# Performance work log

Hardware: AMD Instinct MI355X
Metric: run time of the kernel (lower is better)

Reference implementation:

```python
import jax, jax.numpy as jnp
import numpy as np

E, D, H, K, N = 8, 512, 2048, 2, 1024  # experts, d_model, d_hidden, top_k, tokens
EPS = 1e-5


def _moe_linear(x, idx, W, b):
    # x: (M, in); idx: (M,) expert id per row; W: (E, out, in); b: (E, out)
    # Brute-force: compute per-expert dense GEMMs, select via one-hot (matches
    # BruteForceMoELinear math: y[i] = x[i] @ W[idx[i]].T + b[idx[i]]).
    m = jax.nn.one_hot(idx, W.shape[0], dtype=x.dtype)  # (M, E)
    y = jnp.einsum('me,eoi,mi->mo', m, W, x)
    return y + jnp.take(b, idx, axis=0)


def _forward(inp, gate_w, gate_b, w1, b1, w2, b2, ln_w, ln_b):
    # NaiveGate: linear -> top_k -> softmax over top-k logits
    logits = inp @ gate_w.T + gate_b              # (N, E)
    top_val, top_idx = jax.lax.top_k(logits, K)   # (N, K)
    score = jax.nn.softmax(top_val, axis=-1)      # (N, K)
    # repeat_interleave tokens, dispatch to experts
    x = jnp.repeat(inp, K, axis=0)                # (N*K, D)
    idx = top_idx.reshape(-1)                     # (N*K,)
    x = _moe_linear(x, idx, w1, b1)               # (N*K, H)
    x = jax.nn.gelu(x, approximate=False)         # torch F.gelu default = erf
    x = _moe_linear(x, idx, w2, b2)               # (N*K, D)
    x = x.reshape(N, K, D)
    x = jnp.einsum('nk,nkd->nd', score, x)        # bmm((N,1,K),(N,K,D)) combine
    # post layer norm (pre_lnorm=False)
    mu = jnp.mean(x, axis=-1, keepdims=True)
    var = jnp.var(x, axis=-1, keepdims=True)
    return (x - mu) * jax.lax.rsqrt(var + EPS) * ln_w + ln_b


def setup_inputs() -> dict:
    key = jax.random.key(0)
    ks = jax.random.split(key, 8)
    s = 0.02
    return {
        'inp': jax.random.normal(ks[0], (N, D), dtype=jnp.float32),
        'gate_w': s * jax.random.normal(ks[1], (E, D), dtype=jnp.float32),
        'gate_b': jnp.zeros((E,), dtype=jnp.float32),
        'w1': s * jax.random.normal(ks[2], (E, H, D), dtype=jnp.float32),
        'b1': jnp.zeros((E, H), dtype=jnp.float32),
        'w2': s * jax.random.normal(ks[3], (E, D, H), dtype=jnp.float32),
        'b2': jnp.zeros((E, D), dtype=jnp.float32),
        'ln_w': jnp.ones((D,), dtype=jnp.float32),
        'ln_b': jnp.zeros((D,), dtype=jnp.float32),
    }


def reference(inp, gate_w, gate_b, w1, b1, w2, b2, ln_w, ln_b):
    return _forward(inp, gate_w, gate_b, w1, b1, w2, b2, ln_w, ln_b)
```

## Files before the change

kernel.cpp:

```cpp
#include <hip/hip_runtime.h>
#include <cstdint>
#include <cstddef>

typedef _Float16 half_t;
typedef _Float16 half8 __attribute__((ext_vector_type(8)));
typedef float floatx4 __attribute__((ext_vector_type(4)));

#define E_ 8
#define D_ 512
#define H_ 2048
#define NTOK 1024
#define NP 2048
#define TM 128
#define MAX_TILES 24

__device__ __forceinline__ float gelu_f(float x) {
    return 0.5f * x * (1.0f + erff(x * 0.7071067811865476f));
}

__device__ __forceinline__ void gload_lds16(const half_t* g, half_t* l) {
    __builtin_amdgcn_global_load_lds(
        (__attribute__((address_space(1))) void*)(g),
        (__attribute__((address_space(3))) void*)(l),
        16, 0, 0);
}

__global__ __launch_bounds__(256) void gate_kernel(
        const float* __restrict__ inp, const float* __restrict__ gate_w,
        const float* __restrict__ gate_b, float* __restrict__ logits) {
    int n = blockIdx.x * 4 + (threadIdx.x >> 6);
    int lane = threadIdx.x & 63;
    const floatx4* xr = (const floatx4*)(inp + (size_t)n * D_);
    floatx4 x0 = xr[lane * 2], x1 = xr[lane * 2 + 1];
    #pragma unroll
    for (int e = 0; e < E_; e++) {
        const floatx4* gr = (const floatx4*)(gate_w + (size_t)e * D_);
        floatx4 g0 = gr[lane * 2], g1 = gr[lane * 2 + 1];
        float p = x0[0]*g0[0] + x0[1]*g0[1] + x0[2]*g0[2] + x0[3]*g0[3]
                + x1[0]*g1[0] + x1[1]*g1[1] + x1[2]*g1[2] + x1[3]*g1[3];
        #pragma unroll
        for (int m = 1; m < 64; m <<= 1) p += __shfl_xor(p, m);
        if (lane == 0) logits[(size_t)n * E_ + e] = p + gate_b[e];
    }
}

__global__ __launch_bounds__(256) void plan_kernel(
        const float* __restrict__ logits, float* __restrict__ score,
        int* __restrict__ idx, int* __restrict__ pos_of_pair,
        int* __restrict__ tile_e, int* __restrict__ tile_row0,
        int* __restrict__ tile_cnt, int* __restrict__ ntiles) {
    __shared__ int cnt_s[E_], off_s[E_ + 1], cur_s[E_];
    int tid = threadIdx.x;
    if (tid < E_) { cnt_s[tid] = 0; cur_s[tid] = 0; }
    __syncthreads();
    int my_e[4][2];
    #pragma unroll
    for (int i = 0; i < 4; i++) {
        int n = tid + i * 256;
        float l[E_];
        #pragma unroll
        for (int e = 0; e < E_; e++) l[e] = logits[(size_t)n * E_ + e];
        int e0 = 0; float v0 = l[0];
        #pragma unroll
        for (int e = 1; e < E_; e++) if (l[e] > v0) { v0 = l[e]; e0 = e; }
        int e1 = -1; float v1 = -3.4e38f;
        #pragma unroll
        for (int e = 0; e < E_; e++) if (e != e0 && l[e] > v1) { v1 = l[e]; e1 = e; }
        float s1 = expf(v1 - v0);
        float den = 1.0f + s1;
        score[2 * n]     = 1.0f / den;
        score[2 * n + 1] = s1 / den;
        idx[2 * n]     = e0;
        idx[2 * n + 1] = e1;
        atomicAdd(&cnt_s[e0], 1);
        atomicAdd(&cnt_s[e1], 1);
        my_e[i][0] = e0; my_e[i][1] = e1;
    }
    __syncthreads();
    if (tid == 0) {
        int o = 0;
        #pragma unroll
        for (int e = 0; e < E_; e++) { off_s[e] = o; o += cnt_s[e]; }
        off_s[E_] = o;
        int t = 0;
        for (int e = 0; e < E_; e++) {
            int c = cnt_s[e];
            int nt = (c + TM - 1) / TM;
            for (int i = 0; i < nt; i++) {
                tile_e[t] = e;
                tile_row0[t] = off_s[e] + i * TM;
                int rem = c - i * TM;
                tile_cnt[t] = rem < TM ? rem : TM;
                t++;
            }
        }
        ntiles[0] = t;
    }
    __syncthreads();
    #pragma unroll
    for (int i = 0; i < 4; i++) {
        #pragma unroll
        for (int k = 0; k < 2; k++) {
            int p = (tid + i * 256) * 2 + k;
            int e = my_e[i][k];
            int r = atomicAdd(&cur_s[e], 1);
            pos_of_pair[p] = off_s[e] + r;
        }
    }
}

__global__ __launch_bounds__(256) void scatter_kernel(
        const float* __restrict__ inp, const int* __restrict__ pos_of_pair,
        half_t* __restrict__ Xg) {
    int p = blockIdx.x * 4 + (threadIdx.x >> 6);
    int lane = threadIdx.x & 63;
    int pos = pos_of_pair[p];
    int n = p >> 1;
    const floatx4* src = (const floatx4*)(inp + (size_t)n * D_);
    floatx4 f0 = src[lane * 2], f1 = src[lane * 2 + 1];
    half8 h = { (half_t)f0[0], (half_t)f0[1], (half_t)f0[2], (half_t)f0[3],
                (half_t)f1[0], (half_t)f1[1], (half_t)f1[2], (half_t)f1[3] };
    *(half8*)(Xg + (size_t)pos * D_ + lane * 8) = h;
}

__global__ __launch_bounds__(256) void cvt_kernel(
        const float* __restrict__ w1, const float* __restrict__ w2,
        half_t* __restrict__ W1h, half_t* __restrict__ W2h) {
    const int n8 = E_ * H_ * D_ / 8;
    int i = blockIdx.x * 256 + threadIdx.x;
    const float* src; half_t* dst; int j;
    if (i < n8) { src = w1; dst = W1h; j = i; }
    else        { src = w2; dst = W2h; j = i - n8; }
    const floatx4* s = (const floatx4*)src + (size_t)j * 2;
    floatx4 f0 = s[0], f1 = s[1];
    half8 h = { (half_t)f0[0], (half_t)f0[1], (half_t)f0[2], (half_t)f0[3],
                (half_t)f1[0], (half_t)f1[1], (half_t)f1[2], (half_t)f1[3] };
    *(half8*)(dst + (size_t)j * 8) = h;
}

__global__ __launch_bounds__(256) void gemm1_kernel(
        const half_t* __restrict__ Xg, const half_t* __restrict__ W1h,
        const float* __restrict__ b1,
        const int* __restrict__ tile_e, const int* __restrict__ tile_row0,
        const int* __restrict__ tile_cnt, const int* __restrict__ ntiles,
        half_t* __restrict__ Y1) {
    __shared__ half_t As[TM * 32];
    __shared__ half_t Bs[128 * 32];
    int t = blockIdx.x;
    if (t >= ntiles[0]) return;
    int e = tile_e[t], row0 = tile_row0[t], cnt = tile_cnt[t];
    int colbase = blockIdx.y * 128;
    int tid = threadIdx.x;
    int wave = tid >> 6, lane = tid & 63;
    int quad = lane >> 4, l16 = lane & 15;
    int wm = (wave & 1) * 64, wn = (wave >> 1) * 64;

    int acol = (tid & 3) * 8;
    const half_t* Ag0 = Xg + (size_t)(row0 + (tid >> 2)) * D_ + acol;
    const half_t* Ag1 = Ag0 + 64 * D_;
    const half_t* Bg0 = W1h + ((size_t)e * H_ + colbase + (tid >> 2)) * D_ + acol;
    const half_t* Bg1 = Bg0 + 64 * D_;
    half_t* la0 = As + tid * 8;
    half_t* la1 = As + (tid + 256) * 8;
    half_t* lb0 = Bs + tid * 8;
    half_t* lb1 = Bs + (tid + 256) * 8;

    floatx4 acc[4][4] = {};
    for (int k0 = 0; k0 < D_; k0 += 32) {
        __syncthreads();
        gload_lds16(Ag0 + k0, la0);
        gload_lds16(Ag1 + k0, la1);
        gload_lds16(Bg0 + k0, lb0);
        gload_lds16(Bg1 + k0, lb1);
        __syncthreads();
        half8 a[4], b[4];
        #pragma unroll
        for (int mi = 0; mi < 4; mi++)
            a[mi] = *(const half8*)(As + (wm + mi * 16 + l16) * 32 + quad * 8);
        #pragma unroll
        for (int ni = 0; ni < 4; ni++)
            b[ni] = *(const half8*)(Bs + (wn + ni * 16 + l16) * 32 + quad * 8);
        #pragma unroll
        for (int mi = 0; mi < 4; mi++)
            #pragma unroll
            for (int ni = 0; ni < 4; ni++)
                acc[mi][ni] = __builtin_amdgcn_mfma_f32_16x16x32_f16(a[mi], b[ni], acc[mi][ni], 0, 0, 0);
    }
    float bias[4];
    #pragma unroll
    for (int ni = 0; ni < 4; ni++)
        bias[ni] = b1[(size_t)e * H_ + colbase + wn + ni * 16 + l16];
    #pragma unroll
    for (int mi = 0; mi < 4; mi++) {
        #pragma unroll
        for (int r = 0; r < 4; r++) {
            int rr = wm + mi * 16 + quad * 4 + r;
            if (rr >= cnt) continue;
            size_t rowoff = (size_t)(row0 + rr) * H_;
            #pragma unroll
            for (int ni = 0; ni < 4; ni++) {
                float v = acc[mi][ni][r] + bias[ni];
                Y1[rowoff + colbase + wn + ni * 16 + l16] = (half_t)gelu_f(v);
            }
        }
    }
}

__global__ __launch_bounds__(256) void gemm2_kernel(
        const half_t* __restrict__ Y1, const half_t* __restrict__ W2h,
        const int* __restrict__ tile_e, const int* __restrict__ tile_row0,
        const int* __restrict__ tile_cnt, const int* __restrict__ ntiles,
        float* __restrict__ Y2p) {
    __shared__ half_t As[TM * 32];
    __shared__ half_t Bs[128 * 32];
    int t = blockIdx.x;
    if (t >= ntiles[0]) return;
    int e = tile_e[t], row0 = tile_row0[t], cnt = tile_cnt[t];
    int colbase = blockIdx.y * 128;
    int kz = blockIdx.z;
    int kzbase = kz * 512;
    int tid = threadIdx.x;
    int wave = tid >> 6, lane = tid & 63;
    int quad = lane >> 4, l16 = lane & 15;
    int wm = (wave & 1) * 64, wn = (wave >> 1) * 64;

    int acol = (tid & 3) * 8;
    const half_t* Ag0 = Y1 + (size_t)(row0 + (tid >> 2)) * H_ + kzbase + acol;
    const half_t* Ag1 = Ag0 + 64 * H_;
    const half_t* Bg0 = W2h + ((size_t)e * D_ + colbase + (tid >> 2)) * H_ + kzbase + acol;
    const half_t* Bg1 = Bg0 + 64 * H_;
    half_t* la0 = As + tid * 8;
    half_t* la1 = As + (tid + 256) * 8;
    half_t* lb0 = Bs + tid * 8;
    half_t* lb1 = Bs + (tid + 256) * 8;

    floatx4 acc[4][4] = {};
    for (int k0 = 0; k0 < 512; k0 += 32) {
        __syncthreads();
        gload_lds16(Ag0 + k0, la0);
        gload_lds16(Ag1 + k0, la1);
        gload_lds16(Bg0 + k0, lb0);
        gload_lds16(Bg1 + k0, lb1);
        __syncthreads();
        half8 a[4], b[4];
        #pragma unroll
        for (int mi = 0; mi < 4; mi++)
            a[mi] = *(const half8*)(As + (wm + mi * 16 + l16) * 32 + quad * 8);
        #pragma unroll
        for (int ni = 0; ni < 4; ni++)
            b[ni] = *(const half8*)(Bs + (wn + ni * 16 + l16) * 32 + quad * 8);
        #pragma unroll
        for (int mi = 0; mi < 4; mi++)
            #pragma unroll
            for (int ni = 0; ni < 4; ni++)
                acc[mi][ni] = __builtin_amdgcn_mfma_f32_16x16x32_f16(a[mi], b[ni], acc[mi][ni], 0, 0, 0);
    }
    #pragma unroll
    for (int mi = 0; mi < 4; mi++) {
        #pragma unroll
        for (int r = 0; r < 4; r++) {
            int rr = wm + mi * 16 + quad * 4 + r;
            if (rr >= cnt) continue;
            size_t rowoff = ((size_t)kz * NP + row0 + rr) * D_;
            #pragma unroll
            for (int ni = 0; ni < 4; ni++)
                Y2p[rowoff + colbase + wn + ni * 16 + l16] = acc[mi][ni][r];
        }
    }
}

__global__ __launch_bounds__(256) void final_kernel(
        const float* __restrict__ Y2p, const float* __restrict__ b2,
        const int* __restrict__ idx, const float* __restrict__ score,
        const int* __restrict__ pos_of_pair,
        const float* __restrict__ ln_w, const float* __restrict__ ln_b,
        float* __restrict__ out) {
    int n = blockIdx.x * 4 + (threadIdx.x >> 6);
    int lane = threadIdx.x & 63;
    int p0 = pos_of_pair[2 * n], p1 = pos_of_pair[2 * n + 1];
    int e0 = idx[2 * n], e1 = idx[2 * n + 1];
    float s0 = score[2 * n], s1 = score[2 * n + 1];

    const floatx4* b2r0 = (const floatx4*)(b2 + (size_t)e0 * D_);
    const floatx4* b2r1 = (const floatx4*)(b2 + (size_t)e1 * D_);
    floatx4 a_lo = b2r0[lane * 2], a_hi = b2r0[lane * 2 + 1];
    floatx4 c_lo = b2r1[lane * 2], c_hi = b2r1[lane * 2 + 1];
    #pragma unroll
    for (int kz = 0; kz < 4; kz++) {
        const floatx4* r0 = (const floatx4*)(Y2p + ((size_t)kz * NP + p0) * D_);
        const floatx4* r1 = (const floatx4*)(Y2p + ((size_t)kz * NP + p1) * D_);
        a_lo += r0[lane * 2]; a_hi += r0[lane * 2 + 1];
        c_lo += r1[lane * 2]; c_hi += r1[lane * 2 + 1];
    }
    floatx4 y_lo = s0 * a_lo + s1 * c_lo;
    floatx4 y_hi = s0 * a_hi + s1 * c_hi;

    float s = 0.0f, q = 0.0f;
    #pragma unroll
    for (int j = 0; j < 4; j++) {
        s += y_lo[j] + y_hi[j];
        q += y_lo[j] * y_lo[j] + y_hi[j] * y_hi[j];
    }
    #pragma unroll
    for (int m = 1; m < 64; m <<= 1) {
        s += __shfl_xor(s, m);
        q += __shfl_xor(q, m);
    }
    float mean = s * (1.0f / 512.0f);
    float var = q * (1.0f / 512.0f) - mean * mean;
    float inv = 1.0f / sqrtf(var + 1e-5f);

    const floatx4* wv = (const floatx4*)ln_w;
    const floatx4* bv = (const floatx4*)ln_b;
    floatx4 o_lo = (y_lo - mean) * inv * wv[lane * 2]     + bv[lane * 2];
    floatx4 o_hi = (y_hi - mean) * inv * wv[lane * 2 + 1] + bv[lane * 2 + 1];
    floatx4* op = (floatx4*)(out + (size_t)n * D_);
    op[lane * 2] = o_lo;
    op[lane * 2 + 1] = o_hi;
}

extern "C" void kernel_launch(void* const* d_in, const int* in_sizes, int n_in,
                              void* d_out, int out_size, void* d_ws, size_t ws_size,
                              hipStream_t stream) {
    const float* inp    = (const float*)d_in[0];
    const float* gate_w = (const float*)d_in[1];
    const float* gate_b = (const float*)d_in[2];
    const float* w1     = (const float*)d_in[3];
    const float* b1     = (const float*)d_in[4];
    const float* w2     = (const float*)d_in[5];
    const float* b2     = (const float*)d_in[6];
    const float* ln_w   = (const float*)d_in[7];
    const float* ln_b   = (const float*)d_in[8];
    float* out = (float*)d_out;

    char* ws = (char*)d_ws;
    size_t o = 0;
    auto carve = [&](size_t bytes) -> char* {
        char* p = ws + o;
        o += (bytes + 255) & ~(size_t)255;
        return p;
    };
    half_t* W1h = (half_t*)carve(sizeof(half_t) * (size_t)E_ * H_ * D_);
    half_t* W2h = (half_t*)carve(sizeof(half_t) * (size_t)E_ * D_ * H_);
    half_t* Xg  = (half_t*)carve(sizeof(half_t) * (size_t)(NP + TM) * D_);
    half_t* Y1  = (half_t*)carve(sizeof(half_t) * (size_t)(NP + TM) * H_);
    float*  Y2p = (float*)carve(sizeof(float) * 4 * (size_t)NP * D_);
    float*  logits = (float*)carve(sizeof(float) * NTOK * E_);
    float*  score  = (float*)carve(sizeof(float) * NP);
    int* idx         = (int*)carve(sizeof(int) * NP);
    int* pos_of_pair = (int*)carve(sizeof(int) * NP);
    int* tile_e      = (int*)carve(sizeof(int) * MAX_TILES);
    int* tile_row0   = (int*)carve(sizeof(int) * MAX_TILES);
    int* tile_cnt    = (int*)carve(sizeof(int) * MAX_TILES);
    int* ntiles      = (int*)carve(sizeof(int) * 1);

    gate_kernel<<<NTOK / 4, 256, 0, stream>>>(inp, gate_w, gate_b, logits);
    plan_kernel<<<1, 256, 0, stream>>>(logits, score, idx, pos_of_pair,
                                       tile_e, tile_row0, tile_cnt, ntiles);
    scatter_kernel<<<NP / 4, 256, 0, stream>>>(inp, pos_of_pair, Xg);
    cvt_kernel<<<2 * E_ * H_ * D_ / 8 / 256, 256, 0, stream>>>(w1, w2, W1h, W2h);
    gemm1_kernel<<<dim3(MAX_TILES, H_ / 128), 256, 0, stream>>>(
        Xg, W1h, b1, tile_e, tile_row0, tile_cnt, ntiles, Y1);
    gemm2_kernel<<<dim3(MAX_TILES, D_ / 128, 4), 256, 0, stream>>>(
        Y1, W2h, tile_e, tile_row0, tile_cnt, ntiles, Y2p);
    final_kernel<<<NTOK / 4, 256, 0, stream>>>(Y2p, b2, idx, score, pos_of_pair, ln_w, ln_b, out);
}
```

Measured before the change: 170.1 us.

## Fuse MoE pipeline into one cooperative persistent kernel with grid syncs

Replaces the seven separate launches (gate, plan, scatter, weight conversion, two grouped GEMMs, combine+layernorm) with a single cooperative kernel that loops over work in grid-stride fashion and separates stages with grid.sync(). The gate and top-2 selection are fused per token, and weight conversion runs in the same phase. The GEMM inner loops now stage 64-wide K chunks in doubled LDS buffers, halving the barriers per tile. The aim is to remove launch gaps and tail effects between small kernels, at the cost of grid-wide barrier overhead, a grid capped at 512 blocks, and a single-block planning phase that leaves most CUs idle.

```diff
diff --git a/kernel.cpp b/kernel.cpp
--- a/kernel.cpp
+++ b/kernel.cpp
@@ -1,6 +1,9 @@
 #include <hip/hip_runtime.h>
+#include <hip/hip_cooperative_groups.h>
 #include <cstdint>
 #include <cstddef>
+
+namespace cg = cooperative_groups;
 
 typedef _Float16 half_t;
 typedef _Float16 half8 __attribute__((ext_vector_type(8)));
@@ -14,6 +17,14 @@
 #define TM 128
 #define MAX_TILES 24
 
+struct Params {
+    const float *inp, *gate_w, *gate_b, *w1, *b1, *w2, *b2, *ln_w, *ln_b;
+    float *out;
+    half_t *W1h, *W2h, *Xg, *Y1;
+    float *Y2p, *score;
+    int *idx, *pos, *tile_e, *tile_row0, *tile_cnt, *ntiles;
+};
+
 __device__ __forceinline__ float gelu_f(float x) {
     return 0.5f * x * (1.0f + erff(x * 0.7071067811865476f));
 }
@@ -25,171 +36,51 @@
         16, 0, 0);
 }
 
-__global__ __launch_bounds__(256) void gate_kernel(
-        const float* __restrict__ inp, const float* __restrict__ gate_w,
-        const float* __restrict__ gate_b, float* __restrict__ logits) {
-    int n = blockIdx.x * 4 + (threadIdx.x >> 6);
-    int lane = threadIdx.x & 63;
-    const floatx4* xr = (const floatx4*)(inp + (size_t)n * D_);
-    floatx4 x0 = xr[lane * 2], x1 = xr[lane * 2 + 1];
-    #pragma unroll
-    for (int e = 0; e < E_; e++) {
-        const floatx4* gr = (const floatx4*)(gate_w + (size_t)e * D_);
-        floatx4 g0 = gr[lane * 2], g1 = gr[lane * 2 + 1];
-        float p = x0[0]*g0[0] + x0[1]*g0[1] + x0[2]*g0[2] + x0[3]*g0[3]
-                + x1[0]*g1[0] + x1[1]*g1[1] + x1[2]*g1[2] + x1[3]*g1[3];
-        #pragma unroll
-        for (int m = 1; m < 64; m <<= 1) p += __shfl_xor(p, m);
-        if (lane == 0) logits[(size_t)n * E_ + e] = p + gate_b[e];
-    }
-}
-
-__global__ __launch_bounds__(256) void plan_kernel(
-        const float* __restrict__ logits, float* __restrict__ score,
-        int* __restrict__ idx, int* __restrict__ pos_of_pair,
-        int* __restrict__ tile_e, int* __restrict__ tile_row0,
-        int* __restrict__ tile_cnt, int* __restrict__ ntiles) {
-    __shared__ int cnt_s[E_], off_s[E_ + 1], cur_s[E_];
-    int tid = threadIdx.x;
-    if (tid < E_) { cnt_s[tid] = 0; cur_s[tid] = 0; }
-    __syncthreads();
-    int my_e[4][2];
-    #pragma unroll
-    for (int i = 0; i < 4; i++) {
-        int n = tid + i * 256;
-        float l[E_];
-        #pragma unroll
-        for (int e = 0; e < E_; e++) l[e] = logits[(size_t)n * E_ + e];
-        int e0 = 0; float v0 = l[0];
-        #pragma unroll
-        for (int e = 1; e < E_; e++) if (l[e] > v0) { v0 = l[e]; e0 = e; }
-        int e1 = -1; float v1 = -3.4e38f;
-        #pragma unroll
-        for (int e = 0; e < E_; e++) if (e != e0 && l[e] > v1) { v1 = l[e]; e1 = e; }
-        float s1 = expf(v1 - v0);
-        float den = 1.0f + s1;
-        score[2 * n]     = 1.0f / den;
-        score[2 * n + 1] = s1 / den;
-        idx[2 * n]     = e0;
-        idx[2 * n + 1] = e1;
-        atomicAdd(&cnt_s[e0], 1);
-        atomicAdd(&cnt_s[e1], 1);
-        my_e[i][0] = e0; my_e[i][1] = e1;
-    }
-    __syncthreads();
-    if (tid == 0) {
-        int o = 0;
-        #pragma unroll
-        for (int e = 0; e < E_; e++) { off_s[e] = o; o += cnt_s[e]; }
-        off_s[E_] = o;
-        int t = 0;
-        for (int e = 0; e < E_; e++) {
-            int c = cnt_s[e];
-            int nt = (c + TM - 1) / TM;
-            for (int i = 0; i < nt; i++) {
-                tile_e[t] = e;
-                tile_row0[t] = off_s[e] + i * TM;
-                int rem = c - i * TM;
-                tile_cnt[t] = rem < TM ? rem : TM;
-                t++;
+__device__ void gemm1_job(const Params& P, half_t* As, half_t* Bs,
+                          int t, int cb, int tid) {
+    int e = P.tile_e[t], row0 = P.tile_row0[t], cnt = P.tile_cnt[t];
+    int colbase = cb * 128;
+    int wave = tid >> 6, lane = tid & 63, quad = lane >> 4, l16 = lane & 15;
+    int wm = (wave & 1) * 64, wn = (wave >> 1) * 64;
+    const half_t* Abase = P.Xg + (size_t)row0 * D_;
+    const half_t* Bbase = P.W1h + ((size_t)e * H_ + colbase) * D_;
+    int srow = tid >> 2, scol = (tid & 3) * 8;
+    floatx4 acc[4][4] = {};
+    for (int k0 = 0; k0 < D_; k0 += 64) {
+        __syncthreads();
+        #pragma unroll
+        for (int j = 0; j < 2; j++) {
+            #pragma unroll
+            for (int s = 0; s < 2; s++) {
+                int q = tid + s * 256;
+                int row = srow + s * 64;
+                gload_lds16(Abase + (size_t)row * D_ + k0 + j * 32 + scol,
+                            As + j * 4096 + q * 8);
+                gload_lds16(Bbase + (size_t)row * D_ + k0 + j * 32 + scol,
+                            Bs + j * 4096 + q * 8);
             }
         }
-        ntiles[0] = t;
-    }
-    __syncthreads();
-    #pragma unroll
-    for (int i = 0; i < 4; i++) {
-        #pragma unroll
-        for (int k = 0; k < 2; k++) {
-            int p = (tid + i * 256) * 2 + k;
-            int e = my_e[i][k];
-            int r = atomicAdd(&cur_s[e], 1);
-            pos_of_pair[p] = off_s[e] + r;
-        }
-    }
-}
-
-__global__ __launch_bounds__(256) void scatter_kernel(
-        const float* __restrict__ inp, const int* __restrict__ pos_of_pair,
-        half_t* __restrict__ Xg) {
-    int p = blockIdx.x * 4 + (threadIdx.x >> 6);
-    int lane = threadIdx.x & 63;
-    int pos = pos_of_pair[p];
-    int n = p >> 1;
-    const floatx4* src = (const floatx4*)(inp + (size_t)n * D_);
-    floatx4 f0 = src[lane * 2], f1 = src[lane * 2 + 1];
-    half8 h = { (half_t)f0[0], (half_t)f0[1], (half_t)f0[2], (half_t)f0[3],
-                (half_t)f1[0], (half_t)f1[1], (half_t)f1[2], (half_t)f1[3] };
-    *(half8*)(Xg + (size_t)pos * D_ + lane * 8) = h;
-}
-
-__global__ __launch_bounds__(256) void cvt_kernel(
-        const float* __restrict__ w1, const float* __restrict__ w2,
-        half_t* __restrict__ W1h, half_t* __restrict__ W2h) {
-    const int n8 = E_ * H_ * D_ / 8;
-    int i = blockIdx.x * 256 + threadIdx.x;
-    const float* src; half_t* dst; int j;
-    if (i < n8) { src = w1; dst = W1h; j = i; }
-    else        { src = w2; dst = W2h; j = i - n8; }
-    const floatx4* s = (const floatx4*)src + (size_t)j * 2;
-    floatx4 f0 = s[0], f1 = s[1];
-    half8 h = { (half_t)f0[0], (half_t)f0[1], (half_t)f0[2], (half_t)f0[3],
-                (half_t)f1[0], (half_t)f1[1], (half_t)f1[2], (half_t)f1[3] };
-    *(half8*)(dst + (size_t)j * 8) = h;
-}
-
-__global__ __launch_bounds__(256) void gemm1_kernel(
-        const half_t* __restrict__ Xg, const half_t* __restrict__ W1h,
-        const float* __restrict__ b1,
-        const int* __restrict__ tile_e, const int* __restrict__ tile_row0,
-        const int* __restrict__ tile_cnt, const int* __restrict__ ntiles,
-        half_t* __restrict__ Y1) {
-    __shared__ half_t As[TM * 32];
-    __shared__ half_t Bs[128 * 32];
-    int t = blockIdx.x;
-    if (t >= ntiles[0]) return;
-    int e = tile_e[t], row0 = tile_row0[t], cnt = tile_cnt[t];
-    int colbase = blockIdx.y * 128;
-    int tid = threadIdx.x;
-    int wave = tid >> 6, lane = tid & 63;
-    int quad = lane >> 4, l16 = lane & 15;
-    int wm = (wave & 1) * 64, wn = (wave >> 1) * 64;
-
-    int acol = (tid & 3) * 8;
-    const half_t* Ag0 = Xg + (size_t)(row0 + (tid >> 2)) * D_ + acol;
-    const half_t* Ag1 = Ag0 + 64 * D_;
-    const half_t* Bg0 = W1h + ((size_t)e * H_ + colbase + (tid >> 2)) * D_ + acol;
-    const half_t* Bg1 = Bg0 + 64 * D_;
-    half_t* la0 = As + tid * 8;
-    half_t* la1 = As + (tid + 256) * 8;
-    half_t* lb0 = Bs + tid * 8;
-    half_t* lb1 = Bs + (tid + 256) * 8;
-
-    floatx4 acc[4][4] = {};
-    for (int k0 = 0; k0 < D_; k0 += 32) {
-        __syncthreads();
-        gload_lds16(Ag0 + k0, la0);
-        gload_lds16(Ag1 + k0, la1);
-        gload_lds16(Bg0 + k0, lb0);
-        gload_lds16(Bg1 + k0, lb1);
-        __syncthreads();
-        half8 a[4], b[4];
-        #pragma unroll
-        for (int mi = 0; mi < 4; mi++)
-            a[mi] = *(const half8*)(As + (wm + mi * 16 + l16) * 32 + quad * 8);
-        #pragma unroll
-        for (int ni = 0; ni < 4; ni++)
-            b[ni] = *(const half8*)(Bs + (wn + ni * 16 + l16) * 32 + quad * 8);
-        #pragma unroll
-        for (int mi = 0; mi < 4; mi++)
+        __syncthreads();
+        #pragma unroll
+        for (int j = 0; j < 2; j++) {
+            half8 a[4], b[4];
+            #pragma unroll
+            for (int mi = 0; mi < 4; mi++)
+                a[mi] = *(const half8*)(As + j * 4096 + (wm + mi * 16 + l16) * 32 + quad * 8);
             #pragma unroll
             for (int ni = 0; ni < 4; ni++)
-                acc[mi][ni] = __builtin_amdgcn_mfma_f32_16x16x32_f16(a[mi], b[ni], acc[mi][ni], 0, 0, 0);
+                b[ni] = *(const half8*)(Bs + j * 4096 + (wn + ni * 16 + l16) * 32 + quad * 8);
+            #pragma unroll
+            for (int mi = 0; mi < 4; mi++)
+                #pragma unroll
+                for (int ni = 0; ni < 4; ni++)
+                    acc[mi][ni] = __builtin_amdgcn_mfma_f32_16x16x32_f16(a[mi], b[ni], acc[mi][ni], 0, 0, 0);
+        }
     }
     float bias[4];
     #pragma unroll
     for (int ni = 0; ni < 4; ni++)
-        bias[ni] = b1[(size_t)e * H_ + colbase + wn + ni * 16 + l16];
+        bias[ni] = P.b1[(size_t)e * H_ + colbase + wn + ni * 16 + l16];
     #pragma unroll
     for (int mi = 0; mi < 4; mi++) {
         #pragma unroll
@@ -200,60 +91,53 @@
             #pragma unroll
             for (int ni = 0; ni < 4; ni++) {
                 float v = acc[mi][ni][r] + bias[ni];
-                Y1[rowoff + colbase + wn + ni * 16 + l16] = (half_t)gelu_f(v);
+                P.Y1[rowoff + colbase + wn + ni * 16 + l16] = (half_t)gelu_f(v);
             }
         }
     }
 }
 
-__global__ __launch_bounds__(256) void gemm2_kernel(
-        const half_t* __restrict__ Y1, const half_t* __restrict__ W2h,
-        const int* __restrict__ tile_e, const int* __restrict__ tile_row0,
-        const int* __restrict__ tile_cnt, const int* __restrict__ ntiles,
-        float* __restrict__ Y2p) {
-    __shared__ half_t As[TM * 32];
-    __shared__ half_t Bs[128 * 32];
-    int t = blockIdx.x;
-    if (t >= ntiles[0]) return;
-    int e = tile_e[t], row0 = tile_row0[t], cnt = tile_cnt[t];
-    int colbase = blockIdx.y * 128;
-    int kz = blockIdx.z;
-    int kzbase = kz * 512;
-    int tid = threadIdx.x;
-    int wave = tid >> 6, lane = tid & 63;
-    int quad = lane >> 4, l16 = lane & 15;
+__device__ void gemm2_job(const Params& P, half_t* As, half_t* Bs,
+                          int t, int cb, int kz, int tid) {
+    int e = P.tile_e[t], row0 = P.tile_row0[t], cnt = P.tile_cnt[t];
+    int colbase = cb * 128;
+    int kzb = kz * 512;
+    int wave = tid >> 6, lane = tid & 63, quad = lane >> 4, l16 = lane & 15;
     int wm = (wave & 1) * 64, wn = (wave >> 1) * 64;
-
-    int acol = (tid & 3) * 8;
-    const half_t* Ag0 = Y1 + (size_t)(row0 + (tid >> 2)) * H_ + kzbase + acol;
-    const half_t* Ag1 = Ag0 + 64 * H_;
-    const half_t* Bg0 = W2h + ((size_t)e * D_ + colbase + (tid >> 2)) * H_ + kzbase + acol;
-    const half_t* Bg1 = Bg0 + 64 * H_;
-    half_t* la0 = As + tid * 8;
-    half_t* la1 = As + (tid + 256) * 8;
-    half_t* lb0 = Bs + tid * 8;
-    half_t* lb1 = Bs + (tid + 256) * 8;
-
+    const half_t* Abase = P.Y1 + (size_t)row0 * H_ + kzb;
+    const half_t* Bbase = P.W2h + ((size_t)e * D_ + colbase) * H_ + kzb;
+    int srow = tid >> 2, scol = (tid & 3) * 8;
     floatx4 acc[4][4] = {};
-    for (int k0 = 0; k0 < 512; k0 += 32) {
-        __syncthreads();
-        gload_lds16(Ag0 + k0, la0);
-        gload_lds16(Ag1 + k0, la1);
-        gload_lds16(Bg0 + k0, lb0);
-        gload_lds16(Bg1 + k0, lb1);
-        __syncthreads();
-        half8 a[4], b[4];
-        #pragma unroll
-        for (int mi = 0; mi < 4; mi++)
-            a[mi] = *(const half8*)(As + (wm + mi * 16 + l16) * 32 + quad * 8);
-        #pragma unroll
-        for (int ni = 0; ni < 4; ni++)
-            b[ni] = *(const half8*)(Bs + (wn + ni * 16 + l16) * 32 + quad * 8);
-        #pragma unroll
-        for (int mi = 0; mi < 4; mi++)
+    for (int k0 = 0; k0 < 512; k0 += 64) {
+        __syncthreads();
+        #pragma unroll
+        for (int j = 0; j < 2; j++) {
+            #pragma unroll
+            for (int s = 0; s < 2; s++) {
+                int q = tid + s * 256;
+                int row = srow + s * 64;
+                gload_lds16(Abase + (size_t)row * H_ + k0 + j * 32 + scol,
+                            As + j * 4096 + q * 8);
+                gload_lds16(Bbase + (size_t)row * H_ + k0 + j * 32 + scol,
+                            Bs + j * 4096 + q * 8);
+            }
+        }
+        __syncthreads();
+        #pragma unroll
+        for (int j = 0; j < 2; j++) {
+            half8 a[4], b[4];
+            #pragma unroll
+            for (int mi = 0; mi < 4; mi++)
+                a[mi] = *(const half8*)(As + j * 4096 + (wm + mi * 16 + l16) * 32 + quad * 8);
             #pragma unroll
             for (int ni = 0; ni < 4; ni++)
-                acc[mi][ni] = __builtin_amdgcn_mfma_f32_16x16x32_f16(a[mi], b[ni], acc[mi][ni], 0, 0, 0);
+                b[ni] = *(const half8*)(Bs + j * 4096 + (wn + ni * 16 + l16) * 32 + quad * 8);
+            #pragma unroll
+            for (int mi = 0; mi < 4; mi++)
+                #pragma unroll
+                for (int ni = 0; ni < 4; ni++)
+                    acc[mi][ni] = __builtin_amdgcn_mfma_f32_16x16x32_f16(a[mi], b[ni], acc[mi][ni], 0, 0, 0);
+        }
     }
     #pragma unroll
     for (int mi = 0; mi < 4; mi++) {
@@ -264,75 +148,178 @@
             size_t rowoff = ((size_t)kz * NP + row0 + rr) * D_;
             #pragma unroll
             for (int ni = 0; ni < 4; ni++)
-                Y2p[rowoff + colbase + wn + ni * 16 + l16] = acc[mi][ni][r];
-        }
-    }
-}
-
-__global__ __launch_bounds__(256) void final_kernel(
-        const float* __restrict__ Y2p, const float* __restrict__ b2,
-        const int* __restrict__ idx, const float* __restrict__ score,
-        const int* __restrict__ pos_of_pair,
-        const float* __restrict__ ln_w, const float* __restrict__ ln_b,
-        float* __restrict__ out) {
-    int n = blockIdx.x * 4 + (threadIdx.x >> 6);
-    int lane = threadIdx.x & 63;
-    int p0 = pos_of_pair[2 * n], p1 = pos_of_pair[2 * n + 1];
-    int e0 = idx[2 * n], e1 = idx[2 * n + 1];
-    float s0 = score[2 * n], s1 = score[2 * n + 1];
-
-    const floatx4* b2r0 = (const floatx4*)(b2 + (size_t)e0 * D_);
-    const floatx4* b2r1 = (const floatx4*)(b2 + (size_t)e1 * D_);
-    floatx4 a_lo = b2r0[lane * 2], a_hi = b2r0[lane * 2 + 1];
-    floatx4 c_lo = b2r1[lane * 2], c_hi = b2r1[lane * 2 + 1];
-    #pragma unroll
-    for (int kz = 0; kz < 4; kz++) {
-        const floatx4* r0 = (const floatx4*)(Y2p + ((size_t)kz * NP + p0) * D_);
-        const floatx4* r1 = (const floatx4*)(Y2p + ((size_t)kz * NP + p1) * D_);
-        a_lo += r0[lane * 2]; a_hi += r0[lane * 2 + 1];
-        c_lo += r1[lane * 2]; c_hi += r1[lane * 2 + 1];
-    }
-    floatx4 y_lo = s0 * a_lo + s1 * c_lo;
-    floatx4 y_hi = s0 * a_hi + s1 * c_hi;
-
-    float s = 0.0f, q = 0.0f;
-    #pragma unroll
-    for (int j = 0; j < 4; j++) {
-        s += y_lo[j] + y_hi[j];
-        q += y_lo[j] * y_lo[j] + y_hi[j] * y_hi[j];
-    }
-    #pragma unroll
-    for (int m = 1; m < 64; m <<= 1) {
-        s += __shfl_xor(s, m);
-        q += __shfl_xor(q, m);
-    }
-    float mean = s * (1.0f / 512.0f);
-    float var = q * (1.0f / 512.0f) - mean * mean;
-    float inv = 1.0f / sqrtf(var + 1e-5f);
-
-    const floatx4* wv = (const floatx4*)ln_w;
-    const floatx4* bv = (const floatx4*)ln_b;
-    floatx4 o_lo = (y_lo - mean) * inv * wv[lane * 2]     + bv[lane * 2];
-    floatx4 o_hi = (y_hi - mean) * inv * wv[lane * 2 + 1] + bv[lane * 2 + 1];
-    floatx4* op = (floatx4*)(out + (size_t)n * D_);
-    op[lane * 2] = o_lo;
-    op[lane * 2 + 1] = o_hi;
+                P.Y2p[rowoff + colbase + wn + ni * 16 + l16] = acc[mi][ni][r];
+        }
+    }
+}
+
+__global__ __launch_bounds__(256, 2) void moe_mega(Params P) {
+    cg::grid_group grid = cg::this_grid();
+    __shared__ __align__(16) char smem[32768];
+    half_t* As = (half_t*)smem;
+    half_t* Bs = As + 8192;
+    const int blk = blockIdx.x, tid = threadIdx.x;
+    const int wave = tid >> 6, lane = tid & 63;
+    const int gstride = gridDim.x;
+
+    for (int n = blk * 4 + wave; n < NTOK; n += gstride * 4) {
+        const floatx4* xr = (const floatx4*)(P.inp + (size_t)n * D_);
+        floatx4 x0 = xr[lane * 2], x1 = xr[lane * 2 + 1];
+        float l[E_];
+        #pragma unroll
+        for (int e = 0; e < E_; e++) {
+            const floatx4* gr = (const floatx4*)(P.gate_w + (size_t)e * D_);
+            floatx4 g0 = gr[lane * 2], g1 = gr[lane * 2 + 1];
+            float p = x0[0]*g0[0] + x0[1]*g0[1] + x0[2]*g0[2] + x0[3]*g0[3]
+                    + x1[0]*g1[0] + x1[1]*g1[1] + x1[2]*g1[2] + x1[3]*g1[3];
+            #pragma unroll
+            for (int m = 1; m < 64; m <<= 1) p += __shfl_xor(p, m);
+            l[e] = p + P.gate_b[e];
+        }
+        if (lane == 0) {
+            int e0 = 0; float v0 = l[0];
+            #pragma unroll
+            for (int e = 1; e < E_; e++) if (l[e] > v0) { v0 = l[e]; e0 = e; }
+            int e1 = -1; float v1 = -3.4e38f;
+            #pragma unroll
+            for (int e = 0; e < E_; e++) if (e != e0 && l[e] > v1) { v1 = l[e]; e1 = e; }
+            float s1 = expf(v1 - v0);
+            float den = 1.0f + s1;
+            P.score[2 * n]     = 1.0f / den;
+            P.score[2 * n + 1] = s1 / den;
+            P.idx[2 * n]     = e0;
+            P.idx[2 * n + 1] = e1;
+        }
+    }
+    {
+        const int NG = E_ * H_ * D_ / 8;
+        for (int i = blk * 256 + tid; i < 2 * NG; i += gstride * 256) {
+            const float* src; half_t* dst; int j;
+            if (i < NG) { src = P.w1; dst = P.W1h; j = i; }
+            else        { src = P.w2; dst = P.W2h; j = i - NG; }
+            const floatx4* s = (const floatx4*)src + (size_t)j * 2;
+            floatx4 f0 = s[0], f1 = s[1];
+            half8 h = { (half_t)f0[0], (half_t)f0[1], (half_t)f0[2], (half_t)f0[3],
+                        (half_t)f1[0], (half_t)f1[1], (half_t)f1[2], (half_t)f1[3] };
+            *(half8*)(dst + (size_t)j * 8) = h;
+        }
+    }
+    grid.sync();
+
+    if (blk == 0) {
+        int* cnt_s = (int*)smem;
+        int* off_s = cnt_s + E_;
+        int* cur_s = off_s + E_ + 1;
+        if (tid < E_) { cnt_s[tid] = 0; cur_s[tid] = 0; }
+        __syncthreads();
+        int my_e[8];
+        #pragma unroll
+        for (int i = 0; i < 8; i++) {
+            my_e[i] = P.idx[tid * 8 + i];
+            atomicAdd(&cnt_s[my_e[i]], 1);
+        }
+        __syncthreads();
+        if (tid == 0) {
+            int o = 0;
+            #pragma unroll
+            for (int e = 0; e < E_; e++) { off_s[e] = o; o += cnt_s[e]; }
+            off_s[E_] = o;
+            int t = 0;
+            for (int e = 0; e < E_; e++) {
+                int c = cnt_s[e];
+                int ntt = (c + TM - 1) / TM;
+                for (int i = 0; i < ntt; i++) {
+                    P.tile_e[t] = e;
+                    P.tile_row0[t] = off_s[e] + i * TM;
+                    int rem = c - i * TM;
+                    P.tile_cnt[t] = rem < TM ? rem : TM;
+                    t++;
+                }
+            }
+            P.ntiles[0] = t;
+        }
+        __syncthreads();
+        #pragma unroll
+        for (int i = 0; i < 8; i++) {
+            int e = my_e[i];
+            int r = atomicAdd(&cur_s[e], 1);
+            P.pos[tid * 8 + i] = off_s[e] + r;
+        }
+    }
+    grid.sync();
+
+    for (int p = blk * 4 + wave; p < NP; p += gstride * 4) {
+        int pos = P.pos[p];
+        int n = p >> 1;
+        const floatx4* src = (const floatx4*)(P.inp + (size_t)n * D_);
+        floatx4 f0 = src[lane * 2], f1 = src[lane * 2 + 1];
+        half8 h = { (half_t)f0[0], (half_t)f0[1], (half_t)f0[2], (half_t)f0[3],
+                    (half_t)f1[0], (half_t)f1[1], (half_t)f1[2], (half_t)f1[3] };
+        *(half8*)(P.Xg + (size_t)pos * D_ + lane * 8) = h;
+    }
+    grid.sync();
+
+    {
+        int nt = P.ntiles[0];
+        for (int job = blk; job < nt * 16; job += gstride)
+            gemm1_job(P, As, Bs, job >> 4, job & 15, tid);
+    }
+    grid.sync();
+
+    {
+        int nt = P.ntiles[0];
+        for (int job = blk; job < nt * 16; job += gstride)
+            gemm2_job(P, As, Bs, job >> 4, (job >> 2) & 3, job & 3, tid);
+    }
+    grid.sync();
+
+    for (int n = blk * 4 + wave; n < NTOK; n += gstride * 4) {
+        int p0 = P.pos[2 * n], p1 = P.pos[2 * n + 1];
+        int e0 = P.idx[2 * n], e1 = P.idx[2 * n + 1];
+        float s0 = P.score[2 * n], s1 = P.score[2 * n + 1];
+
+        const floatx4* b2r0 = (const floatx4*)(P.b2 + (size_t)e0 * D_);
+        const floatx4* b2r1 = (const floatx4*)(P.b2 + (size_t)e1 * D_);
+        floatx4 a_lo = b2r0[lane * 2], a_hi = b2r0[lane * 2 + 1];
+        floatx4 c_lo = b2r1[lane * 2], c_hi = b2r1[lane * 2 + 1];
+        #pragma unroll
+        for (int kz = 0; kz < 4; kz++) {
+            const floatx4* r0 = (const floatx4*)(P.Y2p + ((size_t)kz * NP + p0) * D_);
+            const floatx4* r1 = (const floatx4*)(P.Y2p + ((size_t)kz * NP + p1) * D_);
+            a_lo += r0[lane * 2]; a_hi += r0[lane * 2 + 1];
+            c_lo += r1[lane * 2]; c_hi += r1[lane * 2 + 1];
+        }
+        floatx4 y_lo = s0 * a_lo + s1 * c_lo;
+        floatx4 y_hi = s0 * a_hi + s1 * c_hi;
+
+        float s = 0.0f, q = 0.0f;
+        #pragma unroll
+        for (int j = 0; j < 4; j++) {
+            s += y_lo[j] + y_hi[j];
+            q += y_lo[j] * y_lo[j] + y_hi[j] * y_hi[j];
+        }
+        #pragma unroll
+        for (int m = 1; m < 64; m <<= 1) {
+            s += __shfl_xor(s, m);
+            q += __shfl_xor(q, m);
+        }
+        float mean = s * (1.0f / 512.0f);
+        float var = q * (1.0f / 512.0f) - mean * mean;
+        float inv = 1.0f / sqrtf(var + 1e-5f);
+
+        const floatx4* wv = (const floatx4*)P.ln_w;
+        const floatx4* bv = (const floatx4*)P.ln_b;
+        floatx4 o_lo = (y_lo - mean) * inv * wv[lane * 2]     + bv[lane * 2];
+        floatx4 o_hi = (y_hi - mean) * inv * wv[lane * 2 + 1] + bv[lane * 2 + 1];
+        floatx4* op = (floatx4*)(P.out + (size_t)n * D_);
+        op[lane * 2] = o_lo;
+        op[lane * 2 + 1] = o_hi;
+    }
 }
 
 extern "C" void kernel_launch(void* const* d_in, const int* in_sizes, int n_in,
                               void* d_out, int out_size, void* d_ws, size_t ws_size,
                               hipStream_t stream) {
-    const float* inp    = (const float*)d_in[0];
-    const float* gate_w = (const float*)d_in[1];
-    const float* gate_b = (const float*)d_in[2];
-    const float* w1     = (const float*)d_in[3];
-    const float* b1     = (const float*)d_in[4];
-    const float* w2     = (const float*)d_in[5];
-    const float* b2     = (const float*)d_in[6];
-    const float* ln_w   = (const float*)d_in[7];
-    const float* ln_b   = (const float*)d_in[8];
-    float* out = (float*)d_out;
-
     char* ws = (char*)d_ws;
     size_t o = 0;
     auto carve = [&](size_t bytes) -> char* {
@@ -340,28 +327,37 @@
         o += (bytes + 255) & ~(size_t)255;
         return p;
     };
-    half_t* W1h = (half_t*)carve(sizeof(half_t) * (size_t)E_ * H_ * D_);
-    half_t* W2h = (half_t*)carve(sizeof(half_t) * (size_t)E_ * D_ * H_);
-    half_t* Xg  = (half_t*)carve(sizeof(half_t) * (size_t)(NP + TM) * D_);
-    half_t* Y1  = (half_t*)carve(sizeof(half_t) * (size_t)(NP + TM) * H_);
-    float*  Y2p = (float*)carve(sizeof(float) * 4 * (size_t)NP * D_);
-    float*  logits = (float*)carve(sizeof(float) * NTOK * E_);
-    float*  score  = (float*)carve(sizeof(float) * NP);
-    int* idx         = (int*)carve(sizeof(int) * NP);
-    int* pos_of_pair = (int*)carve(sizeof(int) * NP);
-    int* tile_e      = (int*)carve(sizeof(int) * MAX_TILES);
-    int* tile_row0   = (int*)carve(sizeof(int) * MAX_TILES);
-    int* tile_cnt    = (int*)carve(sizeof(int) * MAX_TILES);
-    int* ntiles      = (int*)carve(sizeof(int) * 1);
-
-    gate_kernel<<<NTOK / 4, 256, 0, stream>>>(inp, gate_w, gate_b, logits);
-    plan_kernel<<<1, 256, 0, stream>>>(logits, score, idx, pos_of_pair,
-                                       tile_e, tile_row0, tile_cnt, ntiles);
-    scatter_kernel<<<NP / 4, 256, 0, stream>>>(inp, pos_of_pair, Xg);
-    cvt_kernel<<<2 * E_ * H_ * D_ / 8 / 256, 256, 0, stream>>>(w1, w2, W1h, W2h);
-    gemm1_kernel<<<dim3(MAX_TILES, H_ / 128), 256, 0, stream>>>(
-        Xg, W1h, b1, tile_e, tile_row0, tile_cnt, ntiles, Y1);
-    gemm2_kernel<<<dim3(MAX_TILES, D_ / 128, 4), 256, 0, stream>>>(
-        Y1, W2h, tile_e, tile_row0, tile_cnt, ntiles, Y2p);
-    final_kernel<<<NTOK / 4, 256, 0, stream>>>(Y2p, b2, idx, score, pos_of_pair, ln_w, ln_b, out);
-}
+    Params P;
+    P.inp    = (const float*)d_in[0];
+    P.gate_w = (const float*)d_in[1];
+    P.gate_b = (const float*)d_in[2];
+    P.w1     = (const float*)d_in[3];
+    P.b1     = (const float*)d_in[4];
+    P.w2     = (const float*)d_in[5];
+    P.b2     = (const float*)d_in[6];
+    P.ln_w   = (const float*)d_in[7];
+    P.ln_b   = (const float*)d_in[8];
+    P.out    = (float*)d_out;
+    P.W1h = (half_t*)carve(sizeof(half_t) * (size_t)E_ * H_ * D_);
+    P.W2h = (half_t*)carve(sizeof(half_t) * (size_t)E_ * D_ * H_);
+    P.Xg  = (half_t*)carve(sizeof(half_t) * (size_t)(NP + TM) * D_);
+    P.Y1  = (half_t*)carve(sizeof(half_t) * (size_t)(NP + TM) * H_);
+    P.Y2p = (float*)carve(sizeof(float) * 4 * (size_t)NP * D_);
+    P.score = (float*)carve(sizeof(float) * NP);
+    P.idx   = (int*)carve(sizeof(int) * NP);
+    P.pos   = (int*)carve(sizeof(int) * NP);
+    P.tile_e    = (int*)carve(sizeof(int) * MAX_TILES);
+    P.tile_row0 = (int*)carve(sizeof(int) * MAX_TILES);
+    P.tile_cnt  = (int*)carve(sizeof(int) * MAX_TILES);
+    P.ntiles    = (int*)carve(sizeof(int) * 1);
+
+    int occ = 0;
+    hipOccupancyMaxActiveBlocksPerMultiprocessor(&occ, moe_mega, 256, 0);
+    if (occ < 1) occ = 1;
+    int nblk = occ * 256;
+    if (nblk > 512) nblk = 512;
+
+    void* kp[] = { &P };
+    hipLaunchCooperativeKernel((const void*)moe_mega, dim3(nblk), dim3(256),
+                               kp, 0, stream);
+}
```

Result: slower. 347.1 us (+104.0%).
